# Kernel tuning notes

Measured on AMD Instinct MI355X. Metric: run time of the kernel, lower is better.

The kernel has to match this reference:

```python
import jax, jax.numpy as jnp
import numpy as np

THRESHOLD = 0.2
NEG_POS_RATIO = 3
ALPHA = 1.0
B, M, P, C = 64, 50, 24564, 2


def cxcy_to_xy(c):
    return jnp.concatenate([c[..., :2] - c[..., 2:] / 2, c[..., :2] + c[..., 2:] / 2], axis=-1)


def xy_to_cxcy(x):
    return jnp.concatenate([(x[..., :2] + x[..., 2:]) / 2, x[..., 2:] - x[..., :2]], axis=-1)


def cxcy_to_gcxgcy(c, p):
    # SSD encoding: offsets scaled by 10, sizes (log) scaled by 5
    return jnp.concatenate([(c[..., :2] - p[..., :2]) / (p[..., 2:] / 10.0),
                            jnp.log(c[..., 2:] / p[..., 2:]) * 5.0], axis=-1)


def jaccard(a, b):
    # a: (M,4) xy boxes, b: (P,4) xy boxes -> (M,P) IoU
    lt = jnp.maximum(a[:, None, :2], b[None, :, :2])
    rb = jnp.minimum(a[:, None, 2:], b[None, :, 2:])
    inter = jnp.prod(jnp.clip(rb - lt, 0.0), axis=-1)
    area_a = jnp.prod(a[:, 2:] - a[:, :2], axis=-1)
    area_b = jnp.prod(b[:, 2:] - b[:, :2], axis=-1)
    return inter / (area_a[:, None] + area_b[None, :] - inter)


def setup_inputs() -> dict:
    key = jax.random.key(0)
    k1, k2, k3, k4, k5, k6 = jax.random.split(key, 6)
    predicted_locs = jax.random.normal(k1, (B, P, 4), dtype=jnp.float32)
    predicted_scores = jax.random.normal(k2, (B, P, C), dtype=jnp.float32)
    # valid GT corner boxes in [0,1]: x2>x1, y2>y1
    xy1 = jax.random.uniform(k3, (B, M, 2), minval=0.0, maxval=0.75)
    wh = jax.random.uniform(k4, (B, M, 2), minval=0.05, maxval=0.25)
    boxes = jnp.concatenate([xy1, xy1 + wh], axis=-1).astype(jnp.float32)
    # priors in cxcywh with positive sizes
    pc = jax.random.uniform(k5, (P, 2), minval=0.0, maxval=1.0)
    pwh = jax.random.uniform(k6, (P, 2), minval=0.02, maxval=0.3)
    priors_cxcy = jnp.concatenate([pc, pwh], axis=-1).astype(jnp.float32)
    return {"predicted_locs": predicted_locs, "predicted_scores": predicted_scores,
            "boxes": boxes, "priors_cxcy": priors_cxcy}


def reference(predicted_locs, predicted_scores, boxes, priors_cxcy):
    n_priors = priors_cxcy.shape[0]
    priors_xy = cxcy_to_xy(priors_cxcy)

    def assign(boxes_i):  # boxes_i: (M,4) xy
        overlap = jaccard(boxes_i, priors_xy)  # (M,P)
        overlap_for_each_prior = overlap.max(axis=0)        # (P,)
        object_for_each_prior = overlap.argmax(axis=0)      # (P,)
        prior_for_each_object = overlap.argmax(axis=1)      # (M,)
        # force each object's best prior to be assigned to that object
        object_for_each_prior = object_for_each_prior.at[prior_for_each_object].set(jnp.arange(boxes_i.shape[0]))
        overlap_for_each_prior = overlap_for_each_prior.at[prior_for_each_object].set(1.0)
        labels = jnp.where(overlap_for_each_prior < THRESHOLD, 0, 1).astype(jnp.int32)
        true_locs = cxcy_to_gcxgcy(xy_to_cxcy(boxes_i[object_for_each_prior]), priors_cxcy)
        return labels, true_locs

    true_classes, true_locs = jax.vmap(assign)(boxes)  # (B,P), (B,P,4)
    pos = true_classes != 0                            # (B,P)
    n_pos = pos.sum(axis=1)                            # (B,)
    total_pos = n_pos.sum().astype(jnp.float32)

    # L1Loss(mean) over the positive-prior coordinates
    loc_abs = jnp.abs(predicted_locs - true_locs)
    loc_loss = jnp.sum(loc_abs * pos[..., None]) / (total_pos * 4.0)

    # per-prior cross entropy
    logp = jax.nn.log_softmax(predicted_scores, axis=-1)
    conf_all = -jnp.take_along_axis(logp, true_classes[..., None].astype(jnp.int32), axis=-1)[..., 0]  # (B,P)
    conf_pos_sum = jnp.sum(conf_all * pos)

    # hard negative mining: zero positives, sort descending, take top 3*n_pos per image
    conf_neg = jnp.where(pos, 0.0, conf_all)
    conf_neg_sorted = -jnp.sort(-conf_neg, axis=1)
    ranks = jnp.arange(n_priors)[None, :]
    hard = ranks < (NEG_POS_RATIO * n_pos)[:, None]
    conf_hard_sum = jnp.sum(conf_neg_sorted * hard)

    conf_loss = (conf_hard_sum + conf_pos_sum) / total_pos
    return conf_loss + ALPHA * loc_loss
```

## Files before the change

### kernel.cpp

```cpp
#include <hip/hip_runtime.h>
#include <math.h>

#define BB 64
#define MM 50
#define PP 24564
#define PPT 2
#define NBLK2 48
#define THRESH 0.2f
#define P4 (PP / 4)
#define SLACK 64u
#define NCH 24
#define WMARG 0.151f
#define RCPM 8u
#define SELCH 8
#define SCH4 ((P4 + SELCH - 1) / SELCH)
#define CAP PP

__device__ __forceinline__ float l1loc(float4 bxm, float4 pc, float4 pl) {
    float cx = (bxm.x + bxm.z) * 0.5f, cy = (bxm.y + bxm.w) * 0.5f;
    float w = bxm.z - bxm.x, h = bxm.w - bxm.y;
    float g0 = (cx - pc.x) / (pc.z * 0.1f);
    float g1 = (cy - pc.y) / (pc.w * 0.1f);
    float g2 = logf(w / pc.z) * 5.0f;
    float g3 = logf(h / pc.w) * 5.0f;
    return fabsf(pl.x - g0) + fabsf(pl.y - g1) + fabsf(pl.z - g2) + fabsf(pl.w - g3);
}

__global__ void k_init(int* __restrict__ ghist, int* __restrict__ ghist2,
                       int* __restrict__ gcur, unsigned long long* __restrict__ Lm) {
    int i = blockIdx.x * 256 + threadIdx.x;
    if (i < BB * 2048) ghist[i] = 0;
    if (i < BB * 1024) ghist2[i] = 0;
    if (i < BB) gcur[i] = 0;
    if (i < BB * MM) Lm[i] = 0x00000000FFFFFFFFull;
}

__global__ void k_main(const float4* __restrict__ boxes,
                       const float4* __restrict__ pr_cxcy,
                       const float4* __restrict__ plocs,
                       const float2* __restrict__ scores,
                       unsigned long long* __restrict__ Lm,
                       float* __restrict__ bestv,
                       int* __restrict__ bmv,
                       float* __restrict__ confneg,
                       int* __restrict__ ghist,
                       int* __restrict__ npos_part,
                       float* __restrict__ cpos_part,
                       float* __restrict__ loc_part) {
    int b = blockIdx.y;
    int tid = threadIdx.x;
    int p0 = blockIdx.x * 512 + tid;
    int p1 = p0 + 256;
    bool v0 = (p0 < PP), v1 = (p1 < PP);
    int q0i = v0 ? p0 : PP - 1, q1i = v1 ? p1 : PP - 1;
    __shared__ float4 sbox[MM];
    __shared__ float sarea[MM];
    __shared__ unsigned long long smax[MM];
    __shared__ int shist[2048];
    __shared__ int si[256];
    __shared__ float s1[256], s2[256];
    for (int i = tid; i < 2048; i += 256) shist[i] = 0;
    if (tid < MM) {
        float4 bxt = boxes[b * MM + tid];
        sbox[tid] = bxt;
        sarea[tid] = (bxt.z - bxt.x) * (bxt.w - bxt.y);
        smax[tid] = 0ull;
    }
    __syncthreads();

    float4 pcA = pr_cxcy[q0i], pcB = pr_cxcy[q1i];
    float ax1 = pcA.x - pcA.z * 0.5f, ay1 = pcA.y - pcA.w * 0.5f;
    float ax2 = pcA.x + pcA.z * 0.5f, ay2 = pcA.y + pcA.w * 0.5f;
    float aa = (ax2 - ax1) * (ay2 - ay1);
    float bx1 = pcB.x - pcB.z * 0.5f, by1 = pcB.y - pcB.w * 0.5f;
    float bx2 = pcB.x + pcB.z * 0.5f, by2 = pcB.y + pcB.w * 0.5f;
    float ab = (bx2 - bx1) * (by2 - by1);
    float biA = 0.0f, bdA = 1.0f, biB = 0.0f, bdB = 1.0f;
    int bmA = 0, bmB = 0;
    for (int m = 0; m < MM; ++m) {
        float4 bxm = sbox[m];
        float am = sarea[m];
        {
            float lx = fmaxf(bxm.x, ax1), ly = fmaxf(bxm.y, ay1);
            float rx = fminf(bxm.z, ax2), ry = fminf(bxm.w, ay2);
            float iw = fmaxf(rx - lx, 0.0f), ih = fmaxf(ry - ly, 0.0f);
            float inter = iw * ih;
            float den = am + aa - inter;
            float l = inter * bdA, r = biA * den;
            if (l > r) { biA = inter; bdA = den; bmA = m; }
        }
        {
            float lx = fmaxf(bxm.x, bx1), ly = fmaxf(bxm.y, by1);
            float rx = fminf(bxm.z, bx2), ry = fminf(bxm.w, by2);
            float iw = fmaxf(rx - lx, 0.0f), ih = fmaxf(ry - ly, 0.0f);
            float inter = iw * ih;
            float den = am + ab - inter;
            float l = inter * bdB, r = biB * den;
            if (l > r) { biB = inter; bdB = den; bmB = m; }
        }
    }
    int np = 0;
    float cpos = 0.0f, lloc = 0.0f;
    if (v0) {
        float q = biA / bdA;
        size_t idx = (size_t)b * PP + p0;
        bestv[idx] = q;
        bmv[idx] = bmA;
        unsigned long long key =
            ((unsigned long long)__float_as_uint(q) << 32) | (unsigned int)(~p0);
        atomicMax(&smax[bmA], key);
        bool pos = (q >= THRESH);
        float2 sc = scores[idx];
        float mx = fmaxf(sc.x, sc.y);
        float lse = mx + logf(expf(sc.x - mx) + expf(sc.y - mx));
        float conf = pos ? (lse - sc.y) : (lse - sc.x);
        float ck = pos ? 0.0f : conf;
        confneg[idx] = ck;
        atomicAdd(&shist[__float_as_uint(ck) >> 20], 1);
        if (pos) { np++; cpos += conf; lloc += l1loc(sbox[bmA], pcA, plocs[idx]); }
    }
    if (v1) {
        float q = biB / bdB;
        size_t idx = (size_t)b * PP + p1;
        bestv[idx] = q;
        bmv[idx] = bmB;
        unsigned long long key =
            ((unsigned long long)__float_as_uint(q) << 32) | (unsigned int)(~p1);
        atomicMax(&smax[bmB], key);
        bool pos = (q >= THRESH);
        float2 sc = scores[idx];
        float mx = fmaxf(sc.x, sc.y);
        float lse = mx + logf(expf(sc.x - mx) + expf(sc.y - mx));
        float conf = pos ? (lse - sc.y) : (lse - sc.x);
        float ck = pos ? 0.0f : conf;
        confneg[idx] = ck;
        atomicAdd(&shist[__float_as_uint(ck) >> 20], 1);
        if (pos) { np++; cpos += conf; lloc += l1loc(sbox[bmB], pcB, plocs[idx]); }
    }
    si[tid] = np; s1[tid] = cpos; s2[tid] = lloc;
    __syncthreads();
    for (int s = 128; s > 0; s >>= 1) {
        if (tid < s) {
            si[tid] += si[tid + s];
            s1[tid] += s1[tid + s];
            s2[tid] += s2[tid + s];
        }
        __syncthreads();
    }
    if (tid == 0) {
        int o = b * NBLK2 + blockIdx.x;
        npos_part[o] = si[0];
        cpos_part[o] = s1[0];
        loc_part[o] = s2[0];
    }
    if (tid < MM) {
        unsigned long long v = smax[tid];
        if (v) atomicMax(&Lm[b * MM + tid], v);
    }
    for (int i = tid; i < 2048; i += 256) {
        int c = shist[i];
        if (c) atomicAdd(&ghist[b * 2048 + i], c);
    }
}

__global__ void k_bpo3(const float4* __restrict__ boxes,
                       const float4* __restrict__ pr_cxcy,
                       const float* __restrict__ bestv,
                       unsigned long long* __restrict__ Lm) {
    int b = blockIdx.y, c = blockIdx.x, tid = threadIdx.x;
    __shared__ float4 sbox[MM];
    __shared__ float sarea[MM];
    __shared__ unsigned thr[MM];
    __shared__ unsigned char order[MM];
    __shared__ unsigned long long smax[MM];
    __shared__ unsigned sminthr;
    if (tid < MM) {
        float4 bxt = boxes[b * MM + tid];
        sbox[tid] = bxt;
        sarea[tid] = (bxt.z - bxt.x) * (bxt.w - bxt.y);
        unsigned long long L = Lm[b * MM + tid];
        smax[tid] = L;
        unsigned hi = (unsigned)(L >> 32);
        thr[tid] = (hi > SLACK) ? hi - SLACK : 0u;
    }
    __syncthreads();
    if (tid < MM) {
        unsigned tj = thr[tid];
        int rank = 0;
        for (int k = 0; k < MM; ++k) {
            unsigned tk = thr[k];
            if (tk < tj || (tk == tj && k < tid)) rank++;
        }
        order[rank] = (unsigned char)tid;
    }
    if (tid == 0) {
        unsigned mt = 0xFFFFFFFFu;
        for (int j = 0; j < MM; ++j) mt = min(mt, thr[j]);
        sminthr = mt;
    }
    __syncthreads();
    unsigned minthr = sminthr;
    volatile unsigned long long* vsm = smax;
    const float4* bv4 = (const float4*)(bestv + (size_t)b * PP);
    int i = c * 256 + tid;
    if (i < P4) {
        float4 qv = bv4[i];
        float vv[4] = {qv.x, qv.y, qv.z, qv.w};
        #pragma unroll
        for (int e = 0; e < 4; ++e) {
            unsigned qb = __float_as_uint(vv[e]);
            if (qb < minthr) continue;
            int p = 4 * i + e;
            float4 pc = pr_cxcy[p];
            float px1 = pc.x - pc.z * 0.5f, py1 = pc.y - pc.w * 0.5f;
            float px2 = pc.x + pc.z * 0.5f, py2 = pc.y + pc.w * 0.5f;
            float pa = (px2 - px1) * (py2 - py1);
            for (int jj = 0; jj < MM; ++jj) {
                int j = (int)order[jj];
                if (thr[j] > qb) break;
                float4 bxm = sbox[j];
                if (pc.x < bxm.x - WMARG || pc.x > bxm.z + WMARG ||
                    pc.y < bxm.y - WMARG || pc.y > bxm.w + WMARG) continue;
                float lx = fmaxf(bxm.x, px1), ly = fmaxf(bxm.y, py1);
                float rx = fminf(bxm.z, px2), ry = fminf(bxm.w, py2);
                float iw = fmaxf(rx - lx, 0.0f), ih = fmaxf(ry - ly, 0.0f);
                float inter = iw * ih;
                float den = sarea[j] + pa - inter;
                float qa = inter * __builtin_amdgcn_rcpf(den);
                unsigned hi = (unsigned)(vsm[j] >> 32);
                if (__float_as_uint(qa) + RCPM < hi) continue;
                float q = inter / den;
                unsigned long long key =
                    ((unsigned long long)__float_as_uint(q) << 32) | (unsigned int)(~p);
                if (key > vsm[j]) atomicMax(&smax[j], key);
            }
        }
    }
    __syncthreads();
    if (tid < MM) atomicMax(&Lm[b * MM + tid], smax[tid]);
}

__device__ __forceinline__ float block_sum(float v, float* fred, int tid) {
    fred[tid] = v;
    __syncthreads();
    for (int s = 128; s > 0; s >>= 1) {
        if (tid < s) fred[tid] += fred[tid + s];
        __syncthreads();
    }
    float r = fred[0];
    __syncthreads();
    return r;
}

template <int NB>
__device__ __forceinline__ void suffix_find(const int* __restrict__ h, int K, int tid,
                                            int* iscr, int* bcast, int slot) {
    const int c = NB / 256;
    const int base = tid * c;
    int tsum = 0;
    #pragma unroll
    for (int i = 0; i < c; ++i) tsum += h[base + i];
    iscr[tid] = tsum;
    __syncthreads();
    int val = tsum;
    for (int off = 1; off < 256; off <<= 1) {
        int other = (tid + off < 256) ? iscr[tid + off] : 0;
        __syncthreads();
        val += other;
        iscr[tid] = val;
        __syncthreads();
    }
    int acc = val - tsum;
    int best = -1, cg = 0;
    for (int i = base + c - 1; i >= base; --i) {
        int s = acc + h[i];
        if (s >= K) { best = i; cg = acc; break; }
        acc = s;
    }
    iscr[tid] = best;
    __syncthreads();
    for (int s2 = 128; s2 > 0; s2 >>= 1) {
        if (tid < s2) iscr[tid] = max(iscr[tid], iscr[tid + s2]);
        __syncthreads();
    }
    int gbest = iscr[0];
    __syncthreads();
    if (best == gbest && best >= 0) { bcast[slot] = gbest; bcast[slot + 1] = cg; }
    __syncthreads();
}

__global__ void k_selKF(const float4* __restrict__ boxes,
                        const float4* __restrict__ pr_cxcy,
                        const float4* __restrict__ plocs,
                        const float2* __restrict__ scores,
                        const unsigned long long* __restrict__ Lm,
                        const float* __restrict__ bestv,
                        const int* __restrict__ bmv,
                        float* __restrict__ confneg,
                        const int* __restrict__ ghist,
                        const int* __restrict__ npos_part,
                        int4* __restrict__ selp,
                        int* __restrict__ npfix,
                        float* __restrict__ cposfix,
                        float* __restrict__ llocfix) {
    int b = blockIdx.x, tid = threadIdx.x;
    __shared__ int h[2048];
    __shared__ int iscr[256];
    __shared__ int bcast[8];
    __shared__ int s_dnp;
    for (int i = tid; i < 2048; i += 256) h[i] = ghist[b * 2048 + i];
    __syncthreads();
    if (tid < 64) {
        int fp = -1;
        if (tid < MM) fp = (int)(~(unsigned)(Lm[b * MM + tid] & 0xFFFFFFFFull));
        bool active = (tid < MM);
        for (int m2 = 0; m2 < MM; ++m2) {
            int v = __shfl(fp, m2);
            if (m2 > tid && v == fp) active = false;
        }
        int dnp = 0;
        float dcp = 0.0f, dll = 0.0f;
        if (active) {
            size_t idx = (size_t)b * PP + fp;
            float bo = bestv[idx];
            bool npold = (bo >= THRESH);
            float4 pc = pr_cxcy[fp];
            float4 pl = plocs[idx];
            float llnew = l1loc(boxes[b * MM + tid], pc, pl);
            if (npold) {
                dll = llnew - l1loc(boxes[b * MM + bmv[idx]], pc, pl);
            } else {
                float2 sc = scores[idx];
                float mx = fmaxf(sc.x, sc.y);
                float lse = mx + logf(expf(sc.x - mx) + expf(sc.y - mx));
                dnp = 1;
                dcp = lse - sc.y;
                dll = llnew;
                float cold = confneg[idx];
                atomicAdd(&h[(int)(__float_as_uint(cold) >> 20)], -1);
                atomicAdd(&h[0], 1);
                confneg[idx] = 0.0f;
            }
        }
        #pragma unroll
        for (int off = 32; off > 0; off >>= 1) {
            dnp += __shfl_xor(dnp, off);
            dcp += __shfl_xor(dcp, off);
            dll += __shfl_xor(dll, off);
        }
        if (tid == 0) {
            s_dnp = dnp;
            npfix[b] = dnp; cposfix[b] = dcp; llocfix[b] = dll;
        }
    }
    __syncthreads();
    iscr[tid] = (tid < NBLK2) ? npos_part[b * NBLK2 + tid] : 0;
    __syncthreads();
    for (int s = 128; s > 0; s >>= 1) {
        if (tid < s) iscr[tid] += iscr[tid + s];
        __syncthreads();
    }
    int npos = iscr[0] + s_dnp;
    __syncthreads();
    long long Kl = 3LL * npos;
    int K = (Kl > PP) ? PP : (int)Kl;
    if (K == 0) {
        if (tid == 0) selp[b] = make_int4(0, -1, 0, 0);
        return;
    }
    suffix_find<2048>(h, K, tid, iscr, bcast, 0);
    if (tid == 0) {
        int b1 = bcast[0];
        selp[b] = make_int4(K, b1, K - bcast[1], h[b1]);
    }
}

__global__ void k_selA(const float* __restrict__ confneg,
                       const int4* __restrict__ selp,
                       float* __restrict__ saP,
                       int* __restrict__ ghist2,
                       int* __restrict__ gcur,
                       float* __restrict__ gstore) {
    int b = blockIdx.y, c = blockIdx.x, tid = threadIdx.x;
    __shared__ float fred[256];
    __shared__ int h2[1024];
    __shared__ float sstore[SCH4 * 4];
    __shared__ int scnt, sbase;
    for (int i = tid; i < 1024; i += 256) h2[i] = 0;
    if (tid == 0) scnt = 0;
    __syncthreads();
    int4 sp = selp[b];
    int b1 = sp.y;
    float sa = 0.0f;
    if (b1 >= 0) {
        const float4* cn4 = (const float4*)(confneg + (size_t)b * PP);
        int i1 = min((c + 1) * SCH4, P4);
        for (int i = c * SCH4 + tid; i < i1; i += 256) {
            float4 q = cn4[i];
            float vv[4] = {q.x, q.y, q.z, q.w};
            #pragma unroll
            for (int j = 0; j < 4; ++j) {
                unsigned k = __float_as_uint(vv[j]);
                int t11 = (int)(k >> 20);
                if (t11 > b1) sa += vv[j];
                else if (t11 == b1) {
                    atomicAdd(&h2[(k >> 10) & 1023], 1);
                    int ix = atomicAdd(&scnt, 1);
                    sstore[ix] = vv[j];
                }
            }
        }
    }
    __syncthreads();
    if (tid == 0 && scnt > 0) sbase = atomicAdd(&gcur[b], scnt);
    __syncthreads();
    int n = scnt;
    for (int i = tid; i < n; i += 256)
        gstore[(size_t)b * CAP + sbase + i] = sstore[i];
    for (int i = tid; i < 1024; i += 256) {
        int v = h2[i];
        if (v) atomicAdd(&ghist2[b * 1024 + i], v);
    }
    float Sa = block_sum(sa, fred, tid);
    if (tid == 0) saP[b * SELCH + c] = Sa;
}

__global__ void k_selB(const int4* __restrict__ selp,
                       const float* __restrict__ saP,
                       const int* __restrict__ ghist2,
                       const float* __restrict__ gstore,
                       float* __restrict__ chard) {
    int b = blockIdx.x, tid = threadIdx.x;
    __shared__ int h[1024];
    __shared__ float fred[256];
    __shared__ int iscr[256];
    __shared__ int bcast[8];
    __shared__ float sSa;
    int4 sp = selp[b];
    if (sp.x == 0) {
        if (tid == 0) chard[b] = 0.0f;
        return;
    }
    int b1 = sp.y, K1 = sp.z, h1cnt = sp.w;
    if (tid == 0) {
        float s = 0.0f;
        for (int j = 0; j < SELCH; ++j) s += saP[b * SELCH + j];
        sSa = s;
    }
    for (int i = tid; i < 1024; i += 256) h[i] = ghist2[b * 1024 + i];
    __syncthreads();
    float Sa = sSa;
    suffix_find<1024>(h, K1, tid, iscr, bcast, 0);
    int b2 = bcast[0];
    int K2 = K1 - bcast[1];
    unsigned top21 = ((unsigned)b1 << 10) | (unsigned)b2;
    __syncthreads();

    const float* gs = gstore + (size_t)b * CAP;
    for (int i = tid; i < 1024; i += 256) h[i] = 0;
    __syncthreads();
    float sb = 0.0f;
    for (int i = tid; i < h1cnt; i += 256) {
        float v = gs[i];
        unsigned k = __float_as_uint(v);
        int n10 = (int)((k >> 10) & 1023);
        if (n10 > b2) sb += v;
        else if (n10 == b2) atomicAdd(&h[k & 1023], 1);
    }
    float Sb = block_sum(sb, fred, tid);
    suffix_find<1024>(h, K2, tid, iscr, bcast, 2);
    int b3 = bcast[2];
    int K3 = K2 - bcast[3];
    float sc = 0.0f;
    for (int i = tid; i < h1cnt; i += 256) {
        float v = gs[i];
        unsigned k = __float_as_uint(v);
        if ((k >> 10) == top21 && (k & 1023) > (unsigned)b3) sc += v;
    }
    float Sc = block_sum(sc, fred, tid);
    if (tid == 0) {
        unsigned kstar = (top21 << 10) | (unsigned)b3;
        chard[b] = Sa + Sb + Sc + (float)K3 * __uint_as_float(kstar);
    }
}

__global__ void k_final(const int* __restrict__ npos_part,
                        const float* __restrict__ cpos_part,
                        const float* __restrict__ loc_part,
                        const float* __restrict__ chard,
                        const int* __restrict__ npfix,
                        const float* __restrict__ cposfix,
                        const float* __restrict__ llocfix,
                        float* __restrict__ out) {
    __shared__ int si[256];
    __shared__ float s1[256], s2[256], s3[256];
    int tn = 0; float tc = 0.0f, tl = 0.0f, th = 0.0f;
    for (int i = threadIdx.x; i < BB * NBLK2; i += 256) {
        tn += npos_part[i];
        tc += cpos_part[i];
        tl += loc_part[i];
    }
    if (threadIdx.x < BB) {
        th = chard[threadIdx.x];
        tn += npfix[threadIdx.x];
        tc += cposfix[threadIdx.x];
        tl += llocfix[threadIdx.x];
    }
    si[threadIdx.x] = tn; s1[threadIdx.x] = tc; s2[threadIdx.x] = tl; s3[threadIdx.x] = th;
    __syncthreads();
    for (int s = 128; s > 0; s >>= 1) {
        if (threadIdx.x < s) {
            si[threadIdx.x] += si[threadIdx.x + s];
            s1[threadIdx.x] += s1[threadIdx.x + s];
            s2[threadIdx.x] += s2[threadIdx.x + s];
            s3[threadIdx.x] += s3[threadIdx.x + s];
        }
        __syncthreads();
    }
    if (threadIdx.x == 0) {
        float tp = (float)si[0];
        out[0] = (s3[0] + s1[0]) / tp + s2[0] / (tp * 4.0f);
    }
}

extern "C" void kernel_launch(void* const* d_in, const int* in_sizes, int n_in,
                              void* d_out, int out_size, void* d_ws, size_t ws_size,
                              hipStream_t stream) {
    const float4* plocs   = (const float4*)d_in[0];
    const float2* scores  = (const float2*)d_in[1];
    const float4* boxes   = (const float4*)d_in[2];
    const float4* priors  = (const float4*)d_in[3];
    float* out = (float*)d_out;

    char* ws = (char*)d_ws;
    size_t off = 0;
    auto alloc = [&](size_t bytes) -> void* {
        void* p = ws + off;
        off += (bytes + 255) & ~(size_t)255;
        return p;
    };
    float*              confneg = (float*) alloc((size_t)BB * PP * 4);
    float*              bestv   = (float*) alloc((size_t)BB * PP * 4);
    int*                bmv     = (int*)   alloc((size_t)BB * PP * 4);
    int*                ghist   = (int*)   alloc((size_t)BB * 2048 * 4);
    int*                ghist2  = (int*)   alloc((size_t)BB * 1024 * 4);
    unsigned long long* Lm      = (unsigned long long*)alloc((size_t)BB * MM * 8);
    int*                npos_p  = (int*)   alloc((size_t)BB * NBLK2 * 4);
    float*              cpos_p  = (float*) alloc((size_t)BB * NBLK2 * 4);
    float*              loc_p   = (float*) alloc((size_t)BB * NBLK2 * 4);
    float*              chard   = (float*) alloc((size_t)BB * 4);
    int*                npfix   = (int*)   alloc((size_t)BB * 4);
    float*              cposfix = (float*) alloc((size_t)BB * 4);
    float*              llocfix = (float*) alloc((size_t)BB * 4);
    int4*               selp    = (int4*)  alloc((size_t)BB * 16);
    float*              saP     = (float*) alloc((size_t)BB * SELCH * 4);
    int*                gcur    = (int*)   alloc((size_t)BB * 4);
    float*              gstore  = (float*) alloc((size_t)BB * CAP * 4);
    (void)ws_size; (void)in_sizes; (void)n_in; (void)out_size;

    k_init<<<512, 256, 0, stream>>>(ghist, ghist2, gcur, Lm);
    k_main<<<dim3(NBLK2, BB), 256, 0, stream>>>(boxes, priors, plocs, scores,
                                                Lm, bestv, bmv, confneg, ghist,
                                                npos_p, cpos_p, loc_p);
    k_bpo3<<<dim3(NCH, BB), 256, 0, stream>>>(boxes, priors, bestv, Lm);
    k_selKF<<<BB, 256, 0, stream>>>(boxes, priors, plocs, scores, Lm, bestv, bmv,
                                    confneg, ghist, npos_p, selp,
                                    npfix, cposfix, llocfix);
    k_selA<<<dim3(SELCH, BB), 256, 0, stream>>>(confneg, selp, saP, ghist2, gcur, gstore);
    k_selB<<<BB, 256, 0, stream>>>(selp, saP, ghist2, gstore, chard);
    k_final<<<1, 256, 0, stream>>>(npos_p, cpos_p, loc_p, chard,
                                   npfix, cposfix, llocfix, out);
}
```

Before: 152.1 us.

## Process one prior per thread and read GT boxes from global memory

The main assignment kernel now handles one prior per thread over twice as many blocks, instead of two priors per thread. GT boxes are read directly from global memory (cached) instead of being staged in LDS, and box areas are recomputed inside the loop. The refinement kernel drops the per-box threshold sort and its early break, and instead scans all boxes with a skip test. The aim is more parallelism and less shared-memory setup, at the cost of more global loads, recomputed areas, lost early exit in k_bpo3, and twice as many partial sums to reduce.

```diff
diff --git a/kernel.cpp b/kernel.cpp
--- a/kernel.cpp
+++ b/kernel.cpp
@@ -4,8 +4,7 @@
 #define BB 64
 #define MM 50
 #define PP 24564
-#define PPT 2
-#define NBLK2 48
+#define NBLK 96
 #define THRESH 0.2f
 #define P4 (PP / 4)
 #define SLACK 64u
@@ -48,67 +47,46 @@
                        float* __restrict__ cpos_part,
                        float* __restrict__ loc_part) {
     int b = blockIdx.y;
+    int p = blockIdx.x * 256 + threadIdx.x;
     int tid = threadIdx.x;
-    int p0 = blockIdx.x * 512 + tid;
-    int p1 = p0 + 256;
-    bool v0 = (p0 < PP), v1 = (p1 < PP);
-    int q0i = v0 ? p0 : PP - 1, q1i = v1 ? p1 : PP - 1;
-    __shared__ float4 sbox[MM];
-    __shared__ float sarea[MM];
     __shared__ unsigned long long smax[MM];
     __shared__ int shist[2048];
     __shared__ int si[256];
     __shared__ float s1[256], s2[256];
     for (int i = tid; i < 2048; i += 256) shist[i] = 0;
-    if (tid < MM) {
-        float4 bxt = boxes[b * MM + tid];
-        sbox[tid] = bxt;
-        sarea[tid] = (bxt.z - bxt.x) * (bxt.w - bxt.y);
-        smax[tid] = 0ull;
-    }
-    __syncthreads();
-
-    float4 pcA = pr_cxcy[q0i], pcB = pr_cxcy[q1i];
-    float ax1 = pcA.x - pcA.z * 0.5f, ay1 = pcA.y - pcA.w * 0.5f;
-    float ax2 = pcA.x + pcA.z * 0.5f, ay2 = pcA.y + pcA.w * 0.5f;
-    float aa = (ax2 - ax1) * (ay2 - ay1);
-    float bx1 = pcB.x - pcB.z * 0.5f, by1 = pcB.y - pcB.w * 0.5f;
-    float bx2 = pcB.x + pcB.z * 0.5f, by2 = pcB.y + pcB.w * 0.5f;
-    float ab = (bx2 - bx1) * (by2 - by1);
-    float biA = 0.0f, bdA = 1.0f, biB = 0.0f, bdB = 1.0f;
-    int bmA = 0, bmB = 0;
-    for (int m = 0; m < MM; ++m) {
-        float4 bxm = sbox[m];
-        float am = sarea[m];
-        {
-            float lx = fmaxf(bxm.x, ax1), ly = fmaxf(bxm.y, ay1);
-            float rx = fminf(bxm.z, ax2), ry = fminf(bxm.w, ay2);
+    if (tid < MM) smax[tid] = 0ull;
+    __syncthreads();
+
+    const float4* boxb = boxes + b * MM;
+    int np = 0;
+    float cpos = 0.0f, lloc = 0.0f;
+    if (p < PP) {
+        float4 pc = pr_cxcy[p];
+        float px1 = pc.x - pc.z * 0.5f, py1 = pc.y - pc.w * 0.5f;
+        float px2 = pc.x + pc.z * 0.5f, py2 = pc.y + pc.w * 0.5f;
+        float pa = (px2 - px1) * (py2 - py1);
+        float binter = 0.0f, bdenom = 1.0f;
+        int bm = 0;
+        float4 bbm = boxb[0];
+        #pragma unroll 5
+        for (int m = 0; m < MM; ++m) {
+            float4 bxm = boxb[m];
+            float am = (bxm.z - bxm.x) * (bxm.w - bxm.y);
+            float lx = fmaxf(bxm.x, px1), ly = fmaxf(bxm.y, py1);
+            float rx = fminf(bxm.z, px2), ry = fminf(bxm.w, py2);
             float iw = fmaxf(rx - lx, 0.0f), ih = fmaxf(ry - ly, 0.0f);
             float inter = iw * ih;
-            float den = am + aa - inter;
-            float l = inter * bdA, r = biA * den;
-            if (l > r) { biA = inter; bdA = den; bmA = m; }
-        }
-        {
-            float lx = fmaxf(bxm.x, bx1), ly = fmaxf(bxm.y, by1);
-            float rx = fminf(bxm.z, bx2), ry = fminf(bxm.w, by2);
-            float iw = fmaxf(rx - lx, 0.0f), ih = fmaxf(ry - ly, 0.0f);
-            float inter = iw * ih;
-            float den = am + ab - inter;
-            float l = inter * bdB, r = biB * den;
-            if (l > r) { biB = inter; bdB = den; bmB = m; }
-        }
-    }
-    int np = 0;
-    float cpos = 0.0f, lloc = 0.0f;
-    if (v0) {
-        float q = biA / bdA;
-        size_t idx = (size_t)b * PP + p0;
+            float den = am + pa - inter;
+            float l = inter * bdenom, r = binter * den;
+            if (l > r) { binter = inter; bdenom = den; bm = m; bbm = bxm; }
+        }
+        float q = binter / bdenom;
+        size_t idx = (size_t)b * PP + p;
         bestv[idx] = q;
-        bmv[idx] = bmA;
+        bmv[idx] = bm;
         unsigned long long key =
-            ((unsigned long long)__float_as_uint(q) << 32) | (unsigned int)(~p0);
-        atomicMax(&smax[bmA], key);
+            ((unsigned long long)__float_as_uint(q) << 32) | (unsigned int)(~p);
+        atomicMax(&smax[bm], key);
         bool pos = (q >= THRESH);
         float2 sc = scores[idx];
         float mx = fmaxf(sc.x, sc.y);
@@ -117,25 +95,11 @@
         float ck = pos ? 0.0f : conf;
         confneg[idx] = ck;
         atomicAdd(&shist[__float_as_uint(ck) >> 20], 1);
-        if (pos) { np++; cpos += conf; lloc += l1loc(sbox[bmA], pcA, plocs[idx]); }
-    }
-    if (v1) {
-        float q = biB / bdB;
-        size_t idx = (size_t)b * PP + p1;
-        bestv[idx] = q;
-        bmv[idx] = bmB;
-        unsigned long long key =
-            ((unsigned long long)__float_as_uint(q) << 32) | (unsigned int)(~p1);
-        atomicMax(&smax[bmB], key);
-        bool pos = (q >= THRESH);
-        float2 sc = scores[idx];
-        float mx = fmaxf(sc.x, sc.y);
-        float lse = mx + logf(expf(sc.x - mx) + expf(sc.y - mx));
-        float conf = pos ? (lse - sc.y) : (lse - sc.x);
-        float ck = pos ? 0.0f : conf;
-        confneg[idx] = ck;
-        atomicAdd(&shist[__float_as_uint(ck) >> 20], 1);
-        if (pos) { np++; cpos += conf; lloc += l1loc(sbox[bmB], pcB, plocs[idx]); }
+        if (pos) {
+            np = 1;
+            cpos = conf;
+            lloc = l1loc(bbm, pc, plocs[idx]);
+        }
     }
     si[tid] = np; s1[tid] = cpos; s2[tid] = lloc;
     __syncthreads();
@@ -148,7 +112,7 @@
         __syncthreads();
     }
     if (tid == 0) {
-        int o = b * NBLK2 + blockIdx.x;
+        int o = b * NBLK + blockIdx.x;
         npos_part[o] = si[0];
         cpos_part[o] = s1[0];
         loc_part[o] = s2[0];
@@ -168,31 +132,16 @@
                        const float* __restrict__ bestv,
                        unsigned long long* __restrict__ Lm) {
     int b = blockIdx.y, c = blockIdx.x, tid = threadIdx.x;
-    __shared__ float4 sbox[MM];
-    __shared__ float sarea[MM];
     __shared__ unsigned thr[MM];
-    __shared__ unsigned char order[MM];
     __shared__ unsigned long long smax[MM];
     __shared__ unsigned sminthr;
     if (tid < MM) {
-        float4 bxt = boxes[b * MM + tid];
-        sbox[tid] = bxt;
-        sarea[tid] = (bxt.z - bxt.x) * (bxt.w - bxt.y);
         unsigned long long L = Lm[b * MM + tid];
         smax[tid] = L;
         unsigned hi = (unsigned)(L >> 32);
         thr[tid] = (hi > SLACK) ? hi - SLACK : 0u;
     }
     __syncthreads();
-    if (tid < MM) {
-        unsigned tj = thr[tid];
-        int rank = 0;
-        for (int k = 0; k < MM; ++k) {
-            unsigned tk = thr[k];
-            if (tk < tj || (tk == tj && k < tid)) rank++;
-        }
-        order[rank] = (unsigned char)tid;
-    }
     if (tid == 0) {
         unsigned mt = 0xFFFFFFFFu;
         for (int j = 0; j < MM; ++j) mt = min(mt, thr[j]);
@@ -201,6 +150,7 @@
     __syncthreads();
     unsigned minthr = sminthr;
     volatile unsigned long long* vsm = smax;
+    const float4* boxb = boxes + b * MM;
     const float4* bv4 = (const float4*)(bestv + (size_t)b * PP);
     int i = c * 256 + tid;
     if (i < P4) {
@@ -215,17 +165,17 @@
             float px1 = pc.x - pc.z * 0.5f, py1 = pc.y - pc.w * 0.5f;
             float px2 = pc.x + pc.z * 0.5f, py2 = pc.y + pc.w * 0.5f;
             float pa = (px2 - px1) * (py2 - py1);
-            for (int jj = 0; jj < MM; ++jj) {
-                int j = (int)order[jj];
-                if (thr[j] > qb) break;
-                float4 bxm = sbox[j];
+            for (int j = 0; j < MM; ++j) {
+                if (qb < thr[j]) continue;
+                float4 bxm = boxb[j];
                 if (pc.x < bxm.x - WMARG || pc.x > bxm.z + WMARG ||
                     pc.y < bxm.y - WMARG || pc.y > bxm.w + WMARG) continue;
+                float am = (bxm.z - bxm.x) * (bxm.w - bxm.y);
                 float lx = fmaxf(bxm.x, px1), ly = fmaxf(bxm.y, py1);
                 float rx = fminf(bxm.z, px2), ry = fminf(bxm.w, py2);
                 float iw = fmaxf(rx - lx, 0.0f), ih = fmaxf(ry - ly, 0.0f);
                 float inter = iw * ih;
-                float den = sarea[j] + pa - inter;
+                float den = am + pa - inter;
                 float qa = inter * __builtin_amdgcn_rcpf(den);
                 unsigned hi = (unsigned)(vsm[j] >> 32);
                 if (__float_as_uint(qa) + RCPM < hi) continue;
@@ -354,7 +304,7 @@
         }
     }
     __syncthreads();
-    iscr[tid] = (tid < NBLK2) ? npos_part[b * NBLK2 + tid] : 0;
+    iscr[tid] = (tid < NBLK) ? npos_part[b * NBLK + tid] : 0;
     __syncthreads();
     for (int s = 128; s > 0; s >>= 1) {
         if (tid < s) iscr[tid] += iscr[tid + s];
@@ -495,7 +445,7 @@
     __shared__ int si[256];
     __shared__ float s1[256], s2[256], s3[256];
     int tn = 0; float tc = 0.0f, tl = 0.0f, th = 0.0f;
-    for (int i = threadIdx.x; i < BB * NBLK2; i += 256) {
+    for (int i = threadIdx.x; i < BB * NBLK; i += 256) {
         tn += npos_part[i];
         tc += cpos_part[i];
         tl += loc_part[i];
@@ -545,9 +495,9 @@
     int*                ghist   = (int*)   alloc((size_t)BB * 2048 * 4);
     int*                ghist2  = (int*)   alloc((size_t)BB * 1024 * 4);
     unsigned long long* Lm      = (unsigned long long*)alloc((size_t)BB * MM * 8);
-    int*                npos_p  = (int*)   alloc((size_t)BB * NBLK2 * 4);
-    float*              cpos_p  = (float*) alloc((size_t)BB * NBLK2 * 4);
-    float*              loc_p   = (float*) alloc((size_t)BB * NBLK2 * 4);
+    int*                npos_p  = (int*)   alloc((size_t)BB * NBLK * 4);
+    float*              cpos_p  = (float*) alloc((size_t)BB * NBLK * 4);
+    float*              loc_p   = (float*) alloc((size_t)BB * NBLK * 4);
     float*              chard   = (float*) alloc((size_t)BB * 4);
     int*                npfix   = (int*)   alloc((size_t)BB * 4);
     float*              cposfix = (float*) alloc((size_t)BB * 4);
@@ -559,9 +509,9 @@
     (void)ws_size; (void)in_sizes; (void)n_in; (void)out_size;
 
     k_init<<<512, 256, 0, stream>>>(ghist, ghist2, gcur, Lm);
-    k_main<<<dim3(NBLK2, BB), 256, 0, stream>>>(boxes, priors, plocs, scores,
-                                                Lm, bestv, bmv, confneg, ghist,
-                                                npos_p, cpos_p, loc_p);
+    k_main<<<dim3(NBLK, BB), 256, 0, stream>>>(boxes, priors, plocs, scores,
+                                               Lm, bestv, bmv, confneg, ghist,
+                                               npos_p, cpos_p, loc_p);
     k_bpo3<<<dim3(NCH, BB), 256, 0, stream>>>(boxes, priors, bestv, Lm);
     k_selKF<<<BB, 256, 0, stream>>>(boxes, priors, plocs, scores, Lm, bestv, bmv,
                                     confneg, ghist, npos_p, selp,
```

Result: slower. 156.2 us (+2.7%).
